# Performance work log

Hardware: AMD Instinct MI355X
Metric: run time of the kernel (lower is better)

Reference implementation:

```python
import jax, jax.numpy as jnp
import numpy as np


def setup_inputs() -> dict:
    key = jax.random.key(0)
    kq, kc = jax.random.split(key)
    query = jax.random.normal(kq, (64, 768), dtype=jnp.float32)
    corpus = jax.random.normal(kc, (500000, 768), dtype=jnp.float32)
    return {"query": query, "corpus": corpus, "k": 16}


def reference(query, corpus, k):
    # cosine similarity: (q @ c.T) / (|q|[:,None] * |c|[None,:])  -> [B, N]
    sim = jnp.einsum("bd,nd->bn", query, corpus)
    qn = jnp.linalg.norm(query, axis=1)   # [B]
    cn = jnp.linalg.norm(corpus, axis=1)  # [N]
    sim = sim / (qn[:, None] * cn[None, :])
    # top-k most similar corpus entries per query (largest=True)
    values, indices = jax.lax.top_k(sim, k)  # [B, k], [B, k]
    return values, indices
```

## Files before the change

### kernel.cpp

```cpp
#include <hip/hip_runtime.h>
#include <hip/hip_bf16.h>

#define D 768
#define NQ 64
#define KSTEPS 24
#define SIMB 256
#define SIMT 1024
#define NSIMW (SIMB * 16)
#define NMW 4096
#define NS 8
#define CANDCAP 192
#define MARGIN 1e-3f
#define QLDS_BYTES 98304

typedef float    f32x4 __attribute__((ext_vector_type(4)));
typedef _Float16 h16x8 __attribute__((ext_vector_type(8)));

typedef const void __attribute__((address_space(1)))* gas_ptr;
typedef void __attribute__((address_space(3)))* las_ptr;

__device__ __forceinline__ bool kbetter(float v1, int i1, float v2, int i2) {
    return (v1 > v2) || (v1 == v2 && i1 < i2);
}

__device__ __forceinline__ void topk_insert(float (&tv)[16], int (&ti)[16], float v, int idx) {
    if (!kbetter(v, idx, tv[15], ti[15])) return;
    tv[15] = v; ti[15] = idx;
    #pragma unroll
    for (int s = 15; s >= 1; --s) {
        bool sw = kbetter(tv[s], ti[s], tv[s-1], ti[s-1]);
        float av = sw ? tv[s] : tv[s-1];
        float bv = sw ? tv[s-1] : tv[s];
        int   ai = sw ? ti[s] : ti[s-1];
        int   bi = sw ? ti[s-1] : ti[s];
        tv[s-1] = av; tv[s] = bv; ti[s-1] = ai; ti[s] = bi;
    }
}

__device__ __forceinline__ void bitonic16(float (&v)[16], int (&ix)[16]) {
    #pragma unroll
    for (int d = 8; d >= 1; d >>= 1) {
        #pragma unroll
        for (int i = 0; i < 16; ++i) {
            if ((i & d) == 0) {
                int j = i | d;
                bool sw = kbetter(v[j], ix[j], v[i], ix[i]);
                float av = sw ? v[j] : v[i];
                float bv = sw ? v[i] : v[j];
                int   ai = sw ? ix[j] : ix[i];
                int   bi = sw ? ix[i] : ix[j];
                v[i] = av; v[j] = bv; ix[i] = ai; ix[j] = bi;
            }
        }
    }
}

__device__ __forceinline__ void lane_merge(float (&v)[16], int (&ix)[16], int mask) {
    float pv[16]; int pix[16];
    #pragma unroll
    for (int i = 0; i < 16; ++i) {
        pv[i]  = __shfl_xor(v[15 - i], mask);
        pix[i] = __shfl_xor(ix[15 - i], mask);
    }
    #pragma unroll
    for (int i = 0; i < 16; ++i) {
        if (kbetter(pv[i], pix[i], v[i], ix[i])) { v[i] = pv[i]; ix[i] = pix[i]; }
    }
    bitonic16(v, ix);
}

__device__ __forceinline__ void sort64(float& v, int& ix, int l) {
    #pragma unroll
    for (int k = 2; k <= 64; k <<= 1) {
        #pragma unroll
        for (int j = k >> 1; j >= 1; j >>= 1) {
            float ov = __shfl_xor(v, j);
            int   oi = __shfl_xor(ix, j);
            bool dirDesc = ((l & k) == 0);
            bool lower   = ((l & j) == 0);
            bool takeBetter = (lower == dirDesc);
            bool ob = kbetter(ov, oi, v, ix);
            if (takeBetter == ob) { v = ov; ix = oi; }
        }
    }
}

__device__ __forceinline__ bool kbetterD(double v1, int i1, double v2, int i2) {
    return (v1 > v2) || (v1 == v2 && i1 < i2);
}

__device__ __forceinline__ void topk_insertD(double (&tv)[16], int (&ti)[16], double v, int idx) {
    if (!kbetterD(v, idx, tv[15], ti[15])) return;
    tv[15] = v; ti[15] = idx;
    #pragma unroll
    for (int s = 15; s >= 1; --s) {
        bool sw = kbetterD(tv[s], ti[s], tv[s-1], ti[s-1]);
        double av = sw ? tv[s] : tv[s-1];
        double bv = sw ? tv[s-1] : tv[s];
        int    ai = sw ? ti[s] : ti[s-1];
        int    bi = sw ? ti[s-1] : ti[s];
        tv[s-1] = av; tv[s] = bv; ti[s-1] = ai; ti[s] = bi;
    }
}

__device__ __forceinline__ void bitonic16D(double (&v)[16], int (&ix)[16]) {
    #pragma unroll
    for (int d = 8; d >= 1; d >>= 1) {
        #pragma unroll
        for (int i = 0; i < 16; ++i) {
            if ((i & d) == 0) {
                int j = i | d;
                bool sw = kbetterD(v[j], ix[j], v[i], ix[i]);
                double av = sw ? v[j] : v[i];
                double bv = sw ? v[i] : v[j];
                int    ai = sw ? ix[j] : ix[i];
                int    bi = sw ? ix[i] : ix[j];
                v[i] = av; v[j] = bv; ix[i] = ai; ix[j] = bi;
            }
        }
    }
}

__device__ __forceinline__ void lane_mergeD(double (&v)[16], int (&ix)[16], int mask) {
    double pv[16]; int pix[16];
    #pragma unroll
    for (int i = 0; i < 16; ++i) {
        pv[i]  = __shfl_xor(v[15 - i], mask);
        pix[i] = __shfl_xor(ix[15 - i], mask);
    }
    #pragma unroll
    for (int i = 0; i < 16; ++i) {
        if (kbetterD(pv[i], pix[i], v[i], ix[i])) { v[i] = pv[i]; ix[i] = pix[i]; }
    }
    bitonic16D(v, ix);
}

__global__ __launch_bounds__(256)
void prep_kernel(const float* __restrict__ query, _Float16* __restrict__ qpk,
                 float* __restrict__ qn) {
    int b = blockIdx.x, t = threadIdx.x;
    const float* row = query + b * D;
    float vals[3]; float s = 0.f;
    #pragma unroll
    for (int j = 0; j < 3; ++j) { vals[j] = row[t + 256 * j]; s += vals[j] * vals[j]; }
    #pragma unroll
    for (int m = 1; m < 64; m <<= 1) s += __shfl_xor(s, m);
    __shared__ float ws4[4];
    if ((t & 63) == 0) ws4[t >> 6] = s;
    __syncthreads();
    float qnorm = sqrtf(ws4[0] + ws4[1] + ws4[2] + ws4[3]);
    int qf = b >> 4;
    #pragma unroll
    for (int j = 0; j < 3; ++j) {
        int col = t + 256 * j;
        float vn = vals[j] / qnorm;
        qn[b * D + col] = vn;
        int ks = col >> 5, unit = (col >> 3) & 3, sub = col & 7;
        int lane = (b & 15) + unit * 16;
        qpk[(((size_t)ks * 4 + qf) * 64 + lane) * 8 + sub] = (_Float16)vn;
    }
}

__global__ __launch_bounds__(SIMT, 4)
void sim_kernel(const float* __restrict__ corpus,
                const _Float16* __restrict__ qpk,
                float* __restrict__ simout, int N, int NG16) {
    extern __shared__ __align__(16) char smem[];
    int t = threadIdx.x, w = t >> 6, l = t & 63;
    int n16 = l & 15, kg = l >> 4;

    #pragma unroll
    for (int j = 0; j < 6; ++j) {
        int idx = t + SIMT * j;
        const _Float16* src = qpk + (size_t)idx * 8;
        char* dst = smem + (size_t)idx * 16;
        __builtin_amdgcn_global_load_lds((gas_ptr)(const void*)src, (las_ptr)(void*)dst, 16, 0, 0);
    }
    __syncthreads();
    const _Float16* qlds = (const _Float16*)smem;

    for (int g = blockIdx.x * 16 + w; g < NG16; g += NSIMW) {
        int n = g * 16 + n16;
        int nc = n < N ? n : N - 1;
        const float* pc = corpus + (size_t)nc * D + kg * 8;

        f32x4 acc[4];
        #pragma unroll
        for (int qf = 0; qf < 4; ++qf) acc[qf] = (f32x4)(0.f);
        float ps = 0.f;

        #pragma unroll 4
        for (int ks = 0; ks < KSTEPS; ++ks) {
            f32x4 c0 = *(const f32x4*)(pc + ks * 32);
            f32x4 c1 = *(const f32x4*)(pc + ks * 32 + 4);
            h16x8 hi;
            #pragma unroll
            for (int i = 0; i < 4; ++i) {
                hi[i]     = (_Float16)c0[i];
                hi[4 + i] = (_Float16)c1[i];
                ps += c0[i] * c0[i] + c1[i] * c1[i];
            }
            #pragma unroll
            for (int qf = 0; qf < 4; ++qf) {
                h16x8 qh = *(const h16x8*)(qlds + (((size_t)ks * 4 + qf) * 64 + l) * 8);
                acc[qf] = __builtin_amdgcn_mfma_f32_16x16x32_f16(qh, hi, acc[qf], 0, 0, 0);
            }
        }

        ps += __shfl_xor(ps, 16);
        ps += __shfl_xor(ps, 32);
        float inv = 1.0f / sqrtf(ps);

        if (n < N) {
            float* so = simout + ((size_t)g * 16 + n16) * NQ + kg * 4;
            #pragma unroll
            for (int qf = 0; qf < 4; ++qf) {
                f32x4 v = acc[qf] * inv;
                *(f32x4*)(so + qf * 16) = v;
            }
        }
    }
}

__global__ __launch_bounds__(256)
void mergeA_kernel(const float* __restrict__ simout, float2* __restrict__ candA, int N) {
    int t = threadIdx.x, w = t >> 6, l = t & 63;
    int ww = blockIdx.x * 4 + w;
    int chunk = (N + NMW - 1) / NMW;
    int n0 = ww * chunk, n1 = min(N, n0 + chunk);

    float tv[16]; int ti[16];
    #pragma unroll
    for (int s = 0; s < 16; ++s) { tv[s] = -INFINITY; ti[s] = 0x7fffffff; }

    int n = n0;
    for (; n + 8 <= n1; n += 8) {
        float v[8];
        #pragma unroll
        for (int j = 0; j < 8; ++j) v[j] = simout[(size_t)(n + j) * NQ + l];
        #pragma unroll
        for (int j = 0; j < 8; ++j) topk_insert(tv, ti, v[j], n + j);
    }
    for (; n < n1; ++n) topk_insert(tv, ti, simout[(size_t)n * NQ + l], n);

    float2* dst = candA + ((size_t)l * NMW + ww) * 16;
    #pragma unroll
    for (int s = 0; s < 16; ++s) dst[s] = make_float2(tv[s], __int_as_float(ti[s]));
}

__global__ __launch_bounds__(256)
void merge1_kernel(const float2* __restrict__ cand, float2* __restrict__ cand2, int NWV) {
    int q = blockIdx.x >> 3, seg = blockIdx.x & (NS - 1);
    int t = threadIdx.x, w = t >> 6, l = t & 63;
    int total = NWV * 16;
    int chunk = (total + NS - 1) / NS;
    int e0 = seg * chunk, e1 = min(total, e0 + chunk);
    const float2* src = cand + (size_t)q * total;
    float tv[16]; int ti[16];
    #pragma unroll
    for (int s = 0; s < 16; ++s) { tv[s] = -INFINITY; ti[s] = 0x7fffffff; }
    for (int e = e0 + t; e < e1; e += 256) {
        float2 ce = src[e];
        topk_insert(tv, ti, ce.x, __float_as_int(ce.y));
    }
    lane_merge(tv, ti, 1);  lane_merge(tv, ti, 2);  lane_merge(tv, ti, 4);
    lane_merge(tv, ti, 8);  lane_merge(tv, ti, 16); lane_merge(tv, ti, 32);
    __shared__ float2 stage[64];
    if (l == 0) {
        #pragma unroll
        for (int s = 0; s < 16; ++s) stage[w * 16 + s] = make_float2(tv[s], __int_as_float(ti[s]));
    }
    __syncthreads();
    if (t < 64) {
        float2 ce = stage[t];
        float v = ce.x; int ix = __float_as_int(ce.y);
        sort64(v, ix, t);
        if (t < 16) cand2[((size_t)q * NS + seg) * 16 + t] = make_float2(v, __int_as_float(ix));
    }
}

__global__ __launch_bounds__(64)
void merge2t_kernel(const float2* __restrict__ cand2, float* __restrict__ thr,
                    int* __restrict__ cnt) {
    int q = blockIdx.x, l = threadIdx.x;
    const float2* src = cand2 + (size_t)q * (NS * 16);
    float2 a = src[l], b = src[l + 64];
    float v1 = a.x; int i1 = __float_as_int(a.y);
    float v2 = b.x; int i2 = __float_as_int(b.y);
    sort64(v1, i1, l);
    sort64(v2, i2, l);
    float sv = __shfl(v2, (l - 16) & 63);
    int   si = __shfl(i2, (l - 16) & 63);
    float mv = (l < 16) ? v1 : ((l < 32) ? sv : -INFINITY);
    int   mi = (l < 16) ? i1 : ((l < 32) ? si : 0x7fffffff);
    sort64(mv, mi, l);
    if (l == 15) {
        thr[q] = mv - MARGIN;
        cnt[q] = 0;
    }
}

__global__ __launch_bounds__(256)
void filter_kernel(const float* __restrict__ simout, const float* __restrict__ thr,
                   int* __restrict__ cnt, int* __restrict__ candx, int N) {
    int t = threadIdx.x, w = t >> 6, l = t & 63;
    int wid = blockIdx.x * 4 + w;
    int nwaves = gridDim.x * 4;
    float th = thr[l];
    for (int n = wid; n < N; n += nwaves) {
        float v = simout[(size_t)n * NQ + l];
        if (v >= th) {
            int s = atomicAdd(&cnt[l], 1);
            if (s < CANDCAP) candx[l * CANDCAP + s] = n;
        }
    }
}

__global__ __launch_bounds__(256)
void exact_kernel(const float* __restrict__ corpus, const float* __restrict__ qn,
                  const int* __restrict__ cnt, const int* __restrict__ candx,
                  float* __restrict__ out, int N) {
    int q = blockIdx.x, t = threadIdx.x, w = t >> 6, l = t & 63;
    int m = min(cnt[q], CANDCAP);
    __shared__ double vals[CANDCAP];
    __shared__ int    idxs[CANDCAP];

    const float* qr = qn + q * D;
    for (int c = w; c < m; c += 4) {
        int n = candx[q * CANDCAP + c];
        const float* cr = corpus + (size_t)n * D;
        double acc = 0.0, cs = 0.0;
        #pragma unroll
        for (int j = 0; j < D / 64; ++j) {
            double cv = (double)cr[l + j * 64];
            acc += (double)qr[l + j * 64] * cv;
            cs  += cv * cv;
        }
        #pragma unroll
        for (int msk = 1; msk < 64; msk <<= 1) {
            acc += __shfl_xor(acc, msk);
            cs  += __shfl_xor(cs, msk);
        }
        if (l == 0) { vals[c] = acc / sqrt(cs); idxs[c] = n; }
    }
    __syncthreads();

    if (w == 0) {
        double tv[16]; int ti[16];
        #pragma unroll
        for (int s = 0; s < 16; ++s) { tv[s] = -1e300; ti[s] = 0x7fffffff; }
        for (int r = 0; r < CANDCAP / 64; ++r) {
            int e = l + r * 64;
            if (e < m) topk_insertD(tv, ti, vals[e], idxs[e]);
        }
        lane_mergeD(tv, ti, 1);  lane_mergeD(tv, ti, 2);  lane_mergeD(tv, ti, 4);
        lane_mergeD(tv, ti, 8);  lane_mergeD(tv, ti, 16); lane_mergeD(tv, ti, 32);
        if (l == 0) {
            #pragma unroll
            for (int s = 0; s < 16; ++s) {
                out[q * 16 + s]           = (float)tv[s];
                out[NQ * 16 + q * 16 + s] = (float)ti[s];
            }
        }
    }
}

extern "C" void kernel_launch(void* const* d_in, const int* in_sizes, int n_in,
                              void* d_out, int out_size, void* d_ws, size_t ws_size,
                              hipStream_t stream) {
    const float* query  = (const float*)d_in[0];
    const float* corpus = (const float*)d_in[1];
    int N    = in_sizes[1] / D;
    int NG16 = (N + 15) / 16;

    char* ws = (char*)d_ws;
    _Float16* qpk = (_Float16*)ws;
    float* qn     = (float*)(ws + 98304);
    float* simout = (float*)(ws + 98304 + 196608);
    size_t simBytes = (size_t)NG16 * 16 * NQ * sizeof(float);
    char* p = ws + 98304 + 196608 + simBytes;
    float2* candA = (float2*)p;
    size_t candABytes = (size_t)NQ * NMW * 16 * sizeof(float2);
    float2* cand2 = (float2*)(p + candABytes);
    float*  thr   = (float*)(p + candABytes + 65536);
    int*    cnt   = (int*)(p + candABytes + 65536 + 256);
    int*    candx = (int*)(p + candABytes + 65536 + 512);
    float* out = (float*)d_out;

    (void)hipFuncSetAttribute((const void*)sim_kernel,
                              hipFuncAttributeMaxDynamicSharedMemorySize, QLDS_BYTES);

    prep_kernel<<<NQ, 256, 0, stream>>>(query, qpk, qn);
    sim_kernel<<<SIMB, SIMT, QLDS_BYTES, stream>>>(corpus, qpk, simout, N, NG16);
    mergeA_kernel<<<NMW / 4, 256, 0, stream>>>(simout, candA, N);
    merge1_kernel<<<NQ * NS, 256, 0, stream>>>(candA, cand2, NMW);
    merge2t_kernel<<<NQ, 64, 0, stream>>>(cand2, thr, cnt);
    filter_kernel<<<1024, 256, 0, stream>>>(simout, thr, cnt, candx, N);
    exact_kernel<<<NQ, 256, 0, stream>>>(corpus, qn, cnt, candx, out, N);
}
```

Before: 585.1 us.

## Stage corpus tiles through swizzled LDS with double buffering and store bf16 sims

The similarity kernel is restructured. Each block now walks a contiguous range of 16-row corpus tiles. Threads load a tile into registers, convert it to fp16 and write it into a double-buffered, XOR-swizzled LDS tile while the MFMAs run on the previous tile, and each wave handles one query fragment. The intermediate similarity matrix is stored as bf16 instead of fp32, which halves the write and re-read traffic in the merge and filter passes. To absorb the coarser bf16 values, the filtering margin is widened and the candidate cap raised. This risks candidate overflow, and occupancy drops to 256-thread blocks with large LDS.

```diff
diff --git a/kernel.cpp b/kernel.cpp
--- a/kernel.cpp
+++ b/kernel.cpp
@@ -3,21 +3,32 @@
 
 #define D 768
 #define NQ 64
+#define RT 16
+#define SIMGRID 256
+#define SIMTPB 256
 #define KSTEPS 24
-#define SIMB 256
-#define SIMT 1024
-#define NSIMW (SIMB * 16)
 #define NMW 4096
 #define NS 8
-#define CANDCAP 192
-#define MARGIN 1e-3f
-#define QLDS_BYTES 98304
+#define CANDCAP 256
+#define MARGIN 4e-3f
+
+#define QLDS 98304
+#define CTILE 24576
+#define LDS_BYTES (QLDS + 2 * CTILE + 2 * RT * 4)
 
 typedef float    f32x4 __attribute__((ext_vector_type(4)));
 typedef _Float16 h16x8 __attribute__((ext_vector_type(8)));
 
 typedef const void __attribute__((address_space(1)))* gas_ptr;
 typedef void __attribute__((address_space(3)))* las_ptr;
+
+__device__ __forceinline__ unsigned short f2bf(float f) {
+    unsigned int u = __float_as_uint(f);
+    return (unsigned short)((u + 0x7fffu + ((u >> 16) & 1u)) >> 16);
+}
+__device__ __forceinline__ float bf2f(unsigned short b) {
+    return __uint_as_float(((unsigned int)b) << 16);
+}
 
 __device__ __forceinline__ bool kbetter(float v1, int i1, float v2, int i2) {
     return (v1 > v2) || (v1 == v2 && i1 < i2);
@@ -161,69 +172,95 @@
     }
 }
 
-__global__ __launch_bounds__(SIMT, 4)
+__global__ __launch_bounds__(SIMTPB, 1)
 void sim_kernel(const float* __restrict__ corpus,
                 const _Float16* __restrict__ qpk,
-                float* __restrict__ simout, int N, int NG16) {
+                unsigned short* __restrict__ simout, int N, int NTILES) {
     extern __shared__ __align__(16) char smem[];
+    const _Float16* qlds = (const _Float16*)smem;
+    char*  ct = smem + QLDS;
+    float* cn = (float*)(smem + QLDS + 2 * CTILE);
+
     int t = threadIdx.x, w = t >> 6, l = t & 63;
-    int n16 = l & 15, kg = l >> 4;
-
-    #pragma unroll
-    for (int j = 0; j < 6; ++j) {
-        int idx = t + SIMT * j;
-        const _Float16* src = qpk + (size_t)idx * 8;
-        char* dst = smem + (size_t)idx * 16;
-        __builtin_amdgcn_global_load_lds((gas_ptr)(const void*)src, (las_ptr)(void*)dst, 16, 0, 0);
+    int row = t >> 4, seg = t & 15;
+    int qf = w;
+
+    #pragma unroll
+    for (int j = 0; j < 24; ++j) {
+        int idx = t + 256 * j;
+        __builtin_amdgcn_global_load_lds((gas_ptr)(const void*)(qpk + (size_t)idx * 8),
+                                         (las_ptr)(void*)(smem + (size_t)idx * 16), 16, 0, 0);
     }
     __syncthreads();
-    const _Float16* qlds = (const _Float16*)smem;
-
-    for (int g = blockIdx.x * 16 + w; g < NG16; g += NSIMW) {
-        int n = g * 16 + n16;
-        int nc = n < N ? n : N - 1;
-        const float* pc = corpus + (size_t)nc * D + kg * 8;
-
-        f32x4 acc[4];
-        #pragma unroll
-        for (int qf = 0; qf < 4; ++qf) acc[qf] = (f32x4)(0.f);
+
+    int b = blockIdx.x;
+    int q0 = NTILES / SIMGRID, r0 = NTILES % SIMGRID;
+    int t0 = b * q0 + min(b, r0);
+    int cnt = q0 + (b < r0 ? 1 : 0);
+
+    float4 stg[12];
+
+    auto LOADT = [&](int tile) {
+        long grow = (long)tile * RT + row; if (grow > N - 1) grow = N - 1;
+        const float* p = corpus + (size_t)grow * D + seg * 48;
+        #pragma unroll
+        for (int j = 0; j < 12; ++j) stg[j] = *(const float4*)(p + j * 4);
+    };
+
+    auto CVTW = [&](int buf) {
+        char* base = ct + buf * CTILE;
         float ps = 0.f;
-
-        #pragma unroll 4
+        #pragma unroll
+        for (int j = 0; j < 6; ++j) {
+            float4 a = stg[2 * j], c = stg[2 * j + 1];
+            ps += a.x * a.x + a.y * a.y + a.z * a.z + a.w * a.w;
+            ps += c.x * c.x + c.y * c.y + c.z * c.z + c.w * c.w;
+            h16x8 hv;
+            hv[0] = (_Float16)a.x; hv[1] = (_Float16)a.y; hv[2] = (_Float16)a.z; hv[3] = (_Float16)a.w;
+            hv[4] = (_Float16)c.x; hv[5] = (_Float16)c.y; hv[6] = (_Float16)c.z; hv[7] = (_Float16)c.w;
+            int off = (row * 1536 + seg * 96 + j * 16) ^ ((row & 7) << 4);
+            *(h16x8*)(base + off) = hv;
+        }
+        ps += __shfl_xor(ps, 1); ps += __shfl_xor(ps, 2);
+        ps += __shfl_xor(ps, 4); ps += __shfl_xor(ps, 8);
+        if (seg == 0) cn[buf * RT + row] = ps;
+    };
+
+    auto COMPUTE = [&](int tile, int buf) {
+        const char* base = ct + buf * CTILE;
+        f32x4 acc = (f32x4)(0.f);
+        #pragma unroll
         for (int ks = 0; ks < KSTEPS; ++ks) {
-            f32x4 c0 = *(const f32x4*)(pc + ks * 32);
-            f32x4 c1 = *(const f32x4*)(pc + ks * 32 + 4);
-            h16x8 hi;
-            #pragma unroll
-            for (int i = 0; i < 4; ++i) {
-                hi[i]     = (_Float16)c0[i];
-                hi[4 + i] = (_Float16)c1[i];
-                ps += c0[i] * c0[i] + c1[i] * c1[i];
-            }
-            #pragma unroll
-            for (int qf = 0; qf < 4; ++qf) {
-                h16x8 qh = *(const h16x8*)(qlds + (((size_t)ks * 4 + qf) * 64 + l) * 8);
-                acc[qf] = __builtin_amdgcn_mfma_f32_16x16x32_f16(qh, hi, acc[qf], 0, 0, 0);
-            }
-        }
-
-        ps += __shfl_xor(ps, 16);
-        ps += __shfl_xor(ps, 32);
-        float inv = 1.0f / sqrtf(ps);
-
+            h16x8 qh = *(const h16x8*)(qlds + (((size_t)ks * 4 + qf) * 64 + l) * 8);
+            int cb = ((l & 15) * 1536 + ks * 64 + (l >> 4) * 16) ^ ((l & 7) << 4);
+            h16x8 ch = *(const h16x8*)(base + cb);
+            acc = __builtin_amdgcn_mfma_f32_16x16x32_f16(qh, ch, acc, 0, 0, 0);
+        }
+        int nl = l & 15;
+        long n = (long)tile * RT + nl;
+        float inv = 1.0f / sqrtf(cn[buf * RT + nl]);
         if (n < N) {
-            float* so = simout + ((size_t)g * 16 + n16) * NQ + kg * 4;
-            #pragma unroll
-            for (int qf = 0; qf < 4; ++qf) {
-                f32x4 v = acc[qf] * inv;
-                *(f32x4*)(so + qf * 16) = v;
-            }
-        }
+            ushort4 pk;
+            pk.x = f2bf(acc[0] * inv); pk.y = f2bf(acc[1] * inv);
+            pk.z = f2bf(acc[2] * inv); pk.w = f2bf(acc[3] * inv);
+            *(ushort4*)(simout + n * NQ + qf * 16 + (l >> 4) * 4) = pk;
+        }
+    };
+
+    LOADT(t0);
+    CVTW(0);
+    __syncthreads();
+
+    for (int i = 0; i < cnt; ++i) {
+        if (i + 1 < cnt) LOADT(t0 + i + 1);
+        COMPUTE(t0 + i, i & 1);
+        if (i + 1 < cnt) CVTW((i + 1) & 1);
+        __syncthreads();
     }
 }
 
 __global__ __launch_bounds__(256)
-void mergeA_kernel(const float* __restrict__ simout, float2* __restrict__ candA, int N) {
+void mergeA_kernel(const unsigned short* __restrict__ simout, float2* __restrict__ candA, int N) {
     int t = threadIdx.x, w = t >> 6, l = t & 63;
     int ww = blockIdx.x * 4 + w;
     int chunk = (N + NMW - 1) / NMW;
@@ -237,11 +274,11 @@
     for (; n + 8 <= n1; n += 8) {
         float v[8];
         #pragma unroll
-        for (int j = 0; j < 8; ++j) v[j] = simout[(size_t)(n + j) * NQ + l];
+        for (int j = 0; j < 8; ++j) v[j] = bf2f(simout[(size_t)(n + j) * NQ + l]);
         #pragma unroll
         for (int j = 0; j < 8; ++j) topk_insert(tv, ti, v[j], n + j);
     }
-    for (; n < n1; ++n) topk_insert(tv, ti, simout[(size_t)n * NQ + l], n);
+    for (; n < n1; ++n) topk_insert(tv, ti, bf2f(simout[(size_t)n * NQ + l]), n);
 
     float2* dst = candA + ((size_t)l * NMW + ww) * 16;
     #pragma unroll
@@ -301,14 +338,14 @@
 }
 
 __global__ __launch_bounds__(256)
-void filter_kernel(const float* __restrict__ simout, const float* __restrict__ thr,
+void filter_kernel(const unsigned short* __restrict__ simout, const float* __restrict__ thr,
                    int* __restrict__ cnt, int* __restrict__ candx, int N) {
     int t = threadIdx.x, w = t >> 6, l = t & 63;
     int wid = blockIdx.x * 4 + w;
     int nwaves = gridDim.x * 4;
     float th = thr[l];
     for (int n = wid; n < N; n += nwaves) {
-        float v = simout[(size_t)n * NQ + l];
+        float v = bf2f(simout[(size_t)n * NQ + l]);
         if (v >= th) {
             int s = atomicAdd(&cnt[l], 1);
             if (s < CANDCAP) candx[l * CANDCAP + s] = n;
@@ -370,14 +407,14 @@
                               hipStream_t stream) {
     const float* query  = (const float*)d_in[0];
     const float* corpus = (const float*)d_in[1];
-    int N    = in_sizes[1] / D;
-    int NG16 = (N + 15) / 16;
+    int N      = in_sizes[1] / D;
+    int NTILES = (N + RT - 1) / RT;
 
     char* ws = (char*)d_ws;
     _Float16* qpk = (_Float16*)ws;
     float* qn     = (float*)(ws + 98304);
-    float* simout = (float*)(ws + 98304 + 196608);
-    size_t simBytes = (size_t)NG16 * 16 * NQ * sizeof(float);
+    unsigned short* simout = (unsigned short*)(ws + 98304 + 196608);
+    size_t simBytes = (size_t)NTILES * RT * NQ * sizeof(unsigned short);
     char* p = ws + 98304 + 196608 + simBytes;
     float2* candA = (float2*)p;
     size_t candABytes = (size_t)NQ * NMW * 16 * sizeof(float2);
@@ -388,10 +425,10 @@
     float* out = (float*)d_out;
 
     (void)hipFuncSetAttribute((const void*)sim_kernel,
-                              hipFuncAttributeMaxDynamicSharedMemorySize, QLDS_BYTES);
+                              hipFuncAttributeMaxDynamicSharedMemorySize, LDS_BYTES);
 
     prep_kernel<<<NQ, 256, 0, stream>>>(query, qpk, qn);
-    sim_kernel<<<SIMB, SIMT, QLDS_BYTES, stream>>>(corpus, qpk, simout, N, NG16);
+    sim_kernel<<<SIMGRID, SIMTPB, LDS_BYTES, stream>>>(corpus, qpk, simout, N, NTILES);
     mergeA_kernel<<<NMW / 4, 256, 0, stream>>>(simout, candA, N);
     merge1_kernel<<<NQ * NS, 256, 0, stream>>>(candA, cand2, NMW);
     merge2t_kernel<<<NQ, 64, 0, stream>>>(cand2, thr, cnt);
```

After: 625.9 us. +7.0%, slower.
